# Kernel optimization log

Measured on AMD Instinct MI355X. Metric: run time of the kernel, lower is better.

## Reference

```python
import jax, jax.numpy as jnp
import numpy as np

N, E, G = 20000, 320000, 64
F_IN, H_DIM, HEADS, LAYERS, OUT = 128, 256, 8, 8, 128
HEAD_C = H_DIM // HEADS  # 32
SCALE = 1.0 / np.sqrt(HEAD_C)


def setup_inputs() -> dict:
    key = jax.random.key(0)
    ks = jax.random.split(key, 16)
    s = 0.05
    f32 = jnp.float32
    return {
        "x": jax.random.normal(ks[0], (N, F_IN), f32),
        "edge_index": jax.random.randint(ks[1], (2, E), 0, N),
        "batch": jnp.sort(jax.random.randint(ks[2], (N,), 0, G)),
        "W_init": jax.random.normal(ks[3], (F_IN, H_DIM), f32) * s,
        "b_init": jnp.zeros((H_DIM,), f32),
        "Wq": jax.random.normal(ks[4], (LAYERS, H_DIM, H_DIM), f32) * s,
        "bq": jnp.zeros((LAYERS, H_DIM), f32),
        "Wk": jax.random.normal(ks[5], (LAYERS, H_DIM, H_DIM), f32) * s,
        "bk": jnp.zeros((LAYERS, H_DIM), f32),
        "Wv": jax.random.normal(ks[6], (LAYERS, H_DIM, H_DIM), f32) * s,
        "bv": jnp.zeros((LAYERS, H_DIM), f32),
        "Ws": jax.random.normal(ks[7], (LAYERS, H_DIM, H_DIM), f32) * s,
        "bs": jnp.zeros((LAYERS, H_DIM), f32),
        "Wbeta": jax.random.normal(ks[8], (LAYERS, 3 * H_DIM, 1), f32) * s,
        "ln_g": jnp.ones((LAYERS, H_DIM), f32),
        "ln_b": jnp.zeros((LAYERS, H_DIM), f32),
        "W_final": jax.random.normal(ks[9], (H_DIM, OUT), f32) * s,
        "b_final": jnp.zeros((OUT,), f32),
    }


def _transformer_conv(h, src, dst, Wq, bq, Wk, bk, Wv, bv, Ws, bs, Wbeta):
    # PyG TransformerConv (beta=True, concat=True, eval mode -> no dropout)
    q = (h @ Wq + bq).reshape(N, HEADS, HEAD_C)[dst]   # [E,H,C] query at target
    k = (h @ Wk + bk).reshape(N, HEADS, HEAD_C)[src]   # [E,H,C] key at source
    v = (h @ Wv + bv).reshape(N, HEADS, HEAD_C)[src]   # [E,H,C] value at source
    alpha = jnp.einsum("ehc,ehc->eh", q, k) * SCALE     # [E,H]
    amax = jax.ops.segment_max(alpha, dst, num_segments=N)  # [N,H]
    ex = jnp.exp(alpha - amax[dst])
    denom = jax.ops.segment_sum(ex, dst, num_segments=N)    # [N,H]
    attn = ex / (denom[dst] + 1e-16)                         # [E,H]
    out = jax.ops.segment_sum(v * attn[:, :, None], dst, num_segments=N)
    out = out.reshape(N, H_DIM)
    x_r = h @ Ws + bs                                        # root/skip
    beta = jax.nn.sigmoid(jnp.concatenate([out, x_r, out - x_r], axis=-1) @ Wbeta)  # [N,1]
    return beta * x_r + (1.0 - beta) * out


def _layernorm(x, g, b):
    mu = jnp.mean(x, axis=-1, keepdims=True)
    var = jnp.mean(jnp.square(x - mu), axis=-1, keepdims=True)
    return (x - mu) * jax.lax.rsqrt(var + 1e-5) * g + b


def reference(x, edge_index, batch, W_init, b_init, Wq, bq, Wk, bk, Wv, bv, Ws, bs,
              Wbeta, ln_g, ln_b, W_final, b_final):
    src, dst = edge_index[0], edge_index[1]
    h = x @ W_init + b_init
    for i in range(LAYERS):
        h = _transformer_conv(h, src, dst, Wq[i], bq[i], Wk[i], bk[i],
                              Wv[i], bv[i], Ws[i], bs[i], Wbeta[i])
        h = _layernorm(h, ln_g[i], ln_b[i])
        h = jax.nn.relu(h)
    # global mean pool over graphs
    sums = jax.ops.segment_sum(h, batch, num_segments=G)          # [G,H_DIM]
    cnt = jax.ops.segment_sum(jnp.ones((N,), h.dtype), batch, num_segments=G)
    pooled = sums / jnp.maximum(cnt, 1.0)[:, None]
    return pooled @ W_final + b_final
```

## Files before the change

### kernel.cpp

```cpp
#include <hip/hip_runtime.h>
#include <hip/hip_bf16.h>
#include <math.h>

constexpr int N_NODES  = 20000;
constexpr int M_PAD    = 20096;
constexpr int E_EDGES  = 320000;
constexpr int G_GRAPHS = 64;
constexpr int F_IN     = 128;
constexpr int H_DIM    = 256;
constexpr int LAYERS   = 8;
constexpr float SCALE_ATT = 0.17677669529663687f;

typedef __attribute__((ext_vector_type(8))) short bf16x8;
typedef __attribute__((ext_vector_type(4))) float f32x4;
typedef _Float16 half4 __attribute__((ext_vector_type(4)));
typedef unsigned int u32;

__device__ static inline void gload_lds16(void* lds, const void* g) {
    __builtin_amdgcn_global_load_lds((const __attribute__((address_space(1))) u32*)g,
                                     (__attribute__((address_space(3))) u32*)lds, 16, 0, 0);
}

__global__ void count_kernel(const int* __restrict__ dst, int E, int* __restrict__ counts) {
    int i = blockIdx.x * blockDim.x + threadIdx.x;
    if (i < E) atomicAdd(&counts[dst[i]], 1);
}

__global__ __launch_bounds__(1024) void scan_kernel(const int* __restrict__ counts,
                                                    int* __restrict__ offsets, int n) {
    __shared__ int wsum[16];
    __shared__ int carry_s;
    const int t = threadIdx.x;
    const int lane = t & 63, w = t >> 6;
    if (t == 0) { carry_s = 0; offsets[0] = 0; }
    __syncthreads();
    for (int base = 0; base < n; base += 1024) {
        const int i = base + t;
        const int v = (i < n) ? counts[i] : 0;
        int s = v;
        #pragma unroll
        for (int off = 1; off < 64; off <<= 1) {
            int x = __shfl_up(s, off, 64);
            if (lane >= off) s += x;
        }
        if (lane == 63) wsum[w] = s;
        __syncthreads();
        if (w == 0) {
            int x = (lane < 16) ? wsum[lane] : 0;
            #pragma unroll
            for (int off = 1; off < 16; off <<= 1) {
                int y = __shfl_up(x, off, 64);
                if (lane >= off) x += y;
            }
            if (lane < 16) wsum[lane] = x;
        }
        __syncthreads();
        const int wadd = (w > 0) ? wsum[w - 1] : 0;
        const int inc = carry_s + wadd + s;
        if (i < n) offsets[i + 1] = inc;
        __syncthreads();
        if (t == 1023) carry_s = inc;
        __syncthreads();
    }
}

__global__ void scatter_kernel(const int* __restrict__ src, const int* __restrict__ dst, int E,
                               const int* __restrict__ offsets, int* __restrict__ cursor,
                               int* __restrict__ esrc) {
    int i = blockIdx.x * blockDim.x + threadIdx.x;
    if (i < E) {
        int d = dst[i];
        int pos = atomicAdd(&cursor[d], 1);
        esrc[offsets[d] + pos] = src[i];
    }
}

__global__ __launch_bounds__(256) void wt_layers(
        const float* __restrict__ Wq, const float* __restrict__ Wk,
        const float* __restrict__ Wv, const float* __restrict__ Ws,
        __hip_bfloat16* __restrict__ Whi, __hip_bfloat16* __restrict__ Wlo) {
    const int l = blockIdx.z, z = blockIdx.y;
    const int tk = (blockIdx.x & 7) * 32;
    const int tn = (blockIdx.x >> 3) * 32;
    const float* src = (z == 0 ? Wq : z == 1 ? Wk : z == 2 ? Wv : Ws) + (size_t)l * 65536;
    __shared__ float tile[32][33];
    const int tx = threadIdx.x & 31, ty = threadIdx.x >> 5;
    #pragma unroll
    for (int p = 0; p < 4; ++p)
        tile[ty + p * 8][tx] = src[(size_t)(tk + ty + p * 8) * 256 + tn + tx];
    __syncthreads();
    #pragma unroll
    for (int p = 0; p < 4; ++p) {
        int n = tn + ty + p * 8;
        float v = tile[tx][ty + p * 8];
        size_t o = ((size_t)l * 1024 + z * 256 + n) * 256 + tk + tx;
        __hip_bfloat16 hi = __float2bfloat16(v);
        Whi[o] = hi;
        Wlo[o] = __float2bfloat16(v - __bfloat162float(hi));
    }
}

__global__ __launch_bounds__(256) void wt_init(const float* __restrict__ Wi,
        __hip_bfloat16* __restrict__ Whi, __hip_bfloat16* __restrict__ Wlo) {
    const int tk = (blockIdx.x & 3) * 32;
    const int tn = (blockIdx.x >> 2) * 32;
    __shared__ float tile[32][33];
    const int tx = threadIdx.x & 31, ty = threadIdx.x >> 5;
    #pragma unroll
    for (int p = 0; p < 4; ++p)
        tile[ty + p * 8][tx] = Wi[(size_t)(tk + ty + p * 8) * 256 + tn + tx];
    __syncthreads();
    #pragma unroll
    for (int p = 0; p < 4; ++p) {
        int n = tn + ty + p * 8;
        float v = tile[tx][ty + p * 8];
        size_t o = (size_t)n * 128 + tk + tx;
        __hip_bfloat16 hi = __float2bfloat16(v);
        Whi[o] = hi;
        Wlo[o] = __float2bfloat16(v - __bfloat162float(hi));
    }
}

__global__ __launch_bounds__(256) void bias_cat(const float* __restrict__ bq,
        const float* __restrict__ bk, const float* __restrict__ bv,
        const float* __restrict__ bs, float* __restrict__ bcat) {
    int l = blockIdx.x >> 2, z = blockIdx.x & 3;
    const float* b = (z == 0 ? bq : z == 1 ? bk : z == 2 ? bv : bs) + (size_t)l * 256;
    bcat[(size_t)l * 1024 + z * 256 + threadIdx.x] = b[threadIdx.x];
}

__global__ void conv_hi_lo(const float* __restrict__ src, int n,
                           __hip_bfloat16* __restrict__ hi, __hip_bfloat16* __restrict__ lo) {
    int i = blockIdx.x * blockDim.x + threadIdx.x;
    if (i < n) {
        float v = src[i];
        __hip_bfloat16 h = __float2bfloat16(v);
        hi[i] = h;
        lo[i] = __float2bfloat16(v - __bfloat162float(h));
    }
}

template <int WRITE_MODE>
__global__ __launch_bounds__(256) void gemm_mfma(
        const __hip_bfloat16* __restrict__ Ahi, const __hip_bfloat16* __restrict__ Alo,
        const __hip_bfloat16* __restrict__ Bhi, const __hip_bfloat16* __restrict__ Blo,
        const float* __restrict__ bias, int M, int K,
        float* __restrict__ qs, _Float16* __restrict__ kv,
        __hip_bfloat16* __restrict__ Chi, __hip_bfloat16* __restrict__ Clo) {
    const int t = threadIdx.x;
    const int lane = t & 63, wave = t >> 6;

    const int nwg = gridDim.x * gridDim.y;
    const int lid = blockIdx.y * gridDim.x + blockIdx.x;
    const int qch = nwg >> 3, rch = nwg & 7;
    const int xcd = lid & 7, pos = lid >> 3;
    const int swz = (xcd < rch ? xcd * (qch + 1) : rch * (qch + 1) + (xcd - rch) * qch) + pos;
    const int row0 = (swz / gridDim.x) * 128;
    const int col0 = (swz % gridDim.x) * 128;

    __shared__ __align__(16) __hip_bfloat16 smem[2][4][4096];

    const int ch0 = wave * 64 + lane;
    const int ch1 = ch0 + 256;
    const int rA0 = ch0 >> 2, cA0 = (ch0 & 3) ^ ((rA0 >> 1) & 3);
    const int rA1 = ch1 >> 2, cA1 = (ch1 & 3) ^ ((rA1 >> 1) & 3);
    const size_t gOff0 = (size_t)rA0 * K + cA0 * 8;
    const size_t gOff1 = (size_t)rA1 * K + cA1 * 8;
    const size_t gA0 = (size_t)row0 * K + gOff0, gA1 = (size_t)row0 * K + gOff1;
    const size_t gB0 = (size_t)col0 * K + gOff0, gB1 = (size_t)col0 * K + gOff1;

    const int wr = wave >> 1, wc = wave & 1;
    int offA[4], offB[4];
    #pragma unroll
    for (int f = 0; f < 4; ++f) {
        int ra = wr * 64 + f * 16 + (lane & 15);
        offA[f] = ra * 64 + (((lane >> 4) ^ ((ra >> 1) & 3)) << 4);
        int rb = wc * 64 + f * 16 + (lane & 15);
        offB[f] = rb * 64 + (((lane >> 4) ^ ((rb >> 1) & 3)) << 4);
    }

    f32x4 acc[4][4] = {};
    const int nK = K >> 5;

#define STAGE(BUF, KS) { const size_t ko_ = (size_t)(KS) * 32; \
    gload_lds16((char*)&smem[BUF][0][0] + ch0 * 16, Ahi + gA0 + ko_); \
    gload_lds16((char*)&smem[BUF][0][0] + ch1 * 16, Ahi + gA1 + ko_); \
    gload_lds16((char*)&smem[BUF][1][0] + ch0 * 16, Alo + gA0 + ko_); \
    gload_lds16((char*)&smem[BUF][1][0] + ch1 * 16, Alo + gA1 + ko_); \
    gload_lds16((char*)&smem[BUF][2][0] + ch0 * 16, Bhi + gB0 + ko_); \
    gload_lds16((char*)&smem[BUF][2][0] + ch1 * 16, Bhi + gB1 + ko_); \
    gload_lds16((char*)&smem[BUF][3][0] + ch0 * 16, Blo + gB0 + ko_); \
    gload_lds16((char*)&smem[BUF][3][0] + ch1 * 16, Blo + gB1 + ko_); }

    STAGE(0, 0);
    __syncthreads();
    int cur = 0;
    for (int ks = 0; ks < nK; ++ks) {
        if (ks + 1 < nK) STAGE(cur ^ 1, ks + 1);

        bf16x8 ah[4], al[4], bh[4], bl[4];
        #pragma unroll
        for (int f = 0; f < 4; ++f) {
            ah[f] = *(const bf16x8*)((const char*)&smem[cur][0][0] + offA[f]);
            al[f] = *(const bf16x8*)((const char*)&smem[cur][1][0] + offA[f]);
            bh[f] = *(const bf16x8*)((const char*)&smem[cur][2][0] + offB[f]);
            bl[f] = *(const bf16x8*)((const char*)&smem[cur][3][0] + offB[f]);
        }
        #pragma unroll
        for (int i = 0; i < 4; ++i)
            #pragma unroll
            for (int j = 0; j < 4; ++j) {
                acc[i][j] = __builtin_amdgcn_mfma_f32_16x16x32_bf16(al[i], bh[j], acc[i][j], 0, 0, 0);
                acc[i][j] = __builtin_amdgcn_mfma_f32_16x16x32_bf16(ah[i], bl[j], acc[i][j], 0, 0, 0);
                acc[i][j] = __builtin_amdgcn_mfma_f32_16x16x32_bf16(ah[i], bh[j], acc[i][j], 0, 0, 0);
            }
        __syncthreads();
        cur ^= 1;
    }
#undef STAGE

    const int rb = row0 + wr * 64;
    const int cb = col0 + wc * 64;
    #pragma unroll
    for (int i = 0; i < 4; ++i) {
        #pragma unroll
        for (int j = 0; j < 4; ++j) {
            const int c = cb + j * 16 + (lane & 15);
            const float bz = bias[c];
            #pragma unroll
            for (int rg = 0; rg < 4; ++rg) {
                const int r = rb + i * 16 + (lane >> 4) * 4 + rg;
                if (r < M) {
                    const float v = acc[i][j][rg] + bz;
                    if (WRITE_MODE == 0) {
                        const int sec = c >> 8;
                        if (sec == 0)      qs[(size_t)r * 512 + c] = v * SCALE_ATT;
                        else if (sec == 3) qs[(size_t)r * 512 + c - 512] = v;
                        else               kv[(size_t)r * 512 + c - 256] = (_Float16)v;
                    } else {
                        __hip_bfloat16 hi = __float2bfloat16(v);
                        Chi[(size_t)r * 256 + c] = hi;
                        Clo[(size_t)r * 256 + c] = __float2bfloat16(v - __bfloat162float(hi));
                    }
                }
            }
        }
    }
}

template <int WH>
__global__ __launch_bounds__(256) void node_attn_kernel(
        const float* __restrict__ qs, const _Float16* __restrict__ kv,
        const int* __restrict__ offsets,
        const int* __restrict__ esrc, const float* __restrict__ Wbeta,
        const float* __restrict__ ln_g, const float* __restrict__ ln_b,
        float* __restrict__ h_out,
        __hip_bfloat16* __restrict__ h_hi, __hip_bfloat16* __restrict__ h_lo) {
    const int n = blockIdx.x;
    const int t = threadIdx.x;
    const int lane = t & 63, wave = t >> 6;
    __shared__ int s_src[256];
    __shared__ float s_acc[4][256];
    __shared__ float s_s[4][8];
    __shared__ float red[8];
    __shared__ float s_beta;

    const float4 q4 = reinterpret_cast<const float4*>(qs + (size_t)n * 512)[lane];

    float ssum = 0.f;
    float4 accv = make_float4(0.f, 0.f, 0.f, 0.f);
    const int rs = offsets[n], re = offsets[n + 1];

#define LOADKV(KB, VB, J) { const half4* r_ = reinterpret_cast<const half4*>(kv + (size_t)s_src[(J)] * 512); \
                            KB = r_[lane]; VB = r_[64 + lane]; }
#define STEP(KB, VB) { \
    float p_ = q4.x * (float)KB.x + q4.y * (float)KB.y + q4.z * (float)KB.z + q4.w * (float)KB.w; \
    p_ += __shfl_xor(p_, 1, 8); p_ += __shfl_xor(p_, 2, 8); p_ += __shfl_xor(p_, 4, 8); \
    const float e_ = __expf(p_); \
    ssum += e_; \
    accv.x += e_ * (float)VB.x; \
    accv.y += e_ * (float)VB.y; \
    accv.z += e_ * (float)VB.z; \
    accv.w += e_ * (float)VB.w; }

    for (int base = rs; base < re; base += 256) {
        const int cnt = min(re - base, 256);
        if (t < cnt) s_src[t] = esrc[base + t];
        __syncthreads();

        half4 k0, v0, k1, v1, k2, v2, k3, v3;
        int j = wave;
        if (j      < cnt) LOADKV(k0, v0, j);
        if (j + 4  < cnt) LOADKV(k1, v1, j + 4);
        if (j + 8  < cnt) LOADKV(k2, v2, j + 8);
        if (j + 12 < cnt) LOADKV(k3, v3, j + 12);

        while (j < cnt) {
            STEP(k0, v0); if (j + 16 < cnt) LOADKV(k0, v0, j + 16); j += 4;
            if (j >= cnt) break;
            STEP(k1, v1); if (j + 16 < cnt) LOADKV(k1, v1, j + 16); j += 4;
            if (j >= cnt) break;
            STEP(k2, v2); if (j + 16 < cnt) LOADKV(k2, v2, j + 16); j += 4;
            if (j >= cnt) break;
            STEP(k3, v3); if (j + 16 < cnt) LOADKV(k3, v3, j + 16); j += 4;
        }
        __syncthreads();
    }
#undef LOADKV
#undef STEP

    *reinterpret_cast<float4*>(&s_acc[wave][lane * 4]) = accv;
    if ((lane & 7) == 0) s_s[wave][lane >> 3] = ssum;
    __syncthreads();

    const int hd = t >> 5;
    const float den = s_s[0][hd] + s_s[1][hd] + s_s[2][hd] + s_s[3][hd];
    const float out = (s_acc[0][t] + s_acc[1][t] + s_acc[2][t] + s_acc[3][t]) / (den + 1e-16f);

    const float xr = qs[(size_t)n * 512 + 256 + t];

    float bl = out * (Wbeta[t] + Wbeta[512 + t]) + xr * (Wbeta[256 + t] - Wbeta[512 + t]);
    #pragma unroll
    for (int o = 32; o >= 1; o >>= 1) bl += __shfl_xor(bl, o, 64);
    if ((t & 63) == 0) red[wave] = bl;
    __syncthreads();
    if (t == 0) {
        float v = red[0] + red[1] + red[2] + red[3];
        s_beta = 1.f / (1.f + __expf(-v));
    }
    __syncthreads();
    const float beta = s_beta;
    const float hn = beta * xr + (1.f - beta) * out;

    float r1 = hn;
    #pragma unroll
    for (int o = 32; o >= 1; o >>= 1) r1 += __shfl_xor(r1, o, 64);
    if ((t & 63) == 0) red[4 + wave] = r1;
    __syncthreads();
    const float mu = (red[4] + red[5] + red[6] + red[7]) * (1.f / 256.f);
    const float d = hn - mu;
    float r2 = d * d;
    #pragma unroll
    for (int o = 32; o >= 1; o >>= 1) r2 += __shfl_xor(r2, o, 64);
    if ((t & 63) == 0) red[wave] = r2;
    __syncthreads();
    const float var = (red[0] + red[1] + red[2] + red[3]) * (1.f / 256.f);

    float y = d * rsqrtf(var + 1e-5f) * ln_g[t] + ln_b[t];
    y = fmaxf(y, 0.f);
    if (WH == 1) {
        h_out[(size_t)n * 256 + t] = y;
    } else {
        __hip_bfloat16 hi = __float2bfloat16(y);
        h_hi[(size_t)n * 256 + t] = hi;
        h_lo[(size_t)n * 256 + t] = __float2bfloat16(y - __bfloat162float(hi));
    }
}

constexpr int POOL_N = 32;
__global__ __launch_bounds__(256) void pool_kernel(const float* __restrict__ h,
                                                   const int* __restrict__ batch, int Nn,
                                                   float* __restrict__ sums,
                                                   float* __restrict__ cnt) {
    const int start = blockIdx.x * POOL_N;
    const int end = min(start + POOL_N, Nn);
    if (start >= end) return;
    const int t = threadIdx.x;

    float val[POOL_N];
    #pragma unroll
    for (int i = 0; i < POOL_N; ++i) {
        const int n = start + i;
        val[i] = (n < end) ? h[(size_t)n * 256 + t] : 0.f;
    }

    int cur = batch[start];
    float run = 0.f;
    int c = 0;
    #pragma unroll
    for (int i = 0; i < POOL_N; ++i) {
        const int n = start + i;
        if (n >= end) break;
        const int g = batch[n];
        if (g != cur) {
            atomicAdd(&sums[(size_t)cur * 256 + t], run);
            if (t == 0) atomicAdd(&cnt[cur], (float)c);
            run = 0.f; c = 0; cur = g;
        }
        run += val[i];
        ++c;
    }
    atomicAdd(&sums[(size_t)cur * 256 + t], run);
    if (t == 0) atomicAdd(&cnt[cur], (float)c);
}

__global__ __launch_bounds__(128) void final_kernel(const float* __restrict__ sums,
                                                    const float* __restrict__ cnt,
                                                    const float* __restrict__ Wf,
                                                    const float* __restrict__ bf,
                                                    float* __restrict__ out) {
    const int g = blockIdx.x;
    const int t = threadIdx.x;
    __shared__ float p[256];
    const float c = fmaxf(cnt[g], 1.f);
    for (int i = t; i < 256; i += 128) p[i] = sums[(size_t)g * 256 + i] / c;
    __syncthreads();
    float acc = bf[t];
    #pragma unroll 4
    for (int k = 0; k < 256; ++k) acc += p[k] * Wf[k * 128 + t];
    out[(size_t)g * 128 + t] = acc;
}

extern "C" void kernel_launch(void* const* d_in, const int* in_sizes, int n_in,
                              void* d_out, int out_size, void* d_ws, size_t ws_size,
                              hipStream_t stream) {
    const float* x       = (const float*)d_in[0];
    const int*   eidx    = (const int*)  d_in[1];
    const int*   batch   = (const int*)  d_in[2];
    const float* W_init  = (const float*)d_in[3];
    const float* b_init  = (const float*)d_in[4];
    const float* Wq      = (const float*)d_in[5];
    const float* bq      = (const float*)d_in[6];
    const float* Wk      = (const float*)d_in[7];
    const float* bk      = (const float*)d_in[8];
    const float* Wv      = (const float*)d_in[9];
    const float* bv      = (const float*)d_in[10];
    const float* Ws      = (const float*)d_in[11];
    const float* bs      = (const float*)d_in[12];
    const float* Wbeta   = (const float*)d_in[13];
    const float* ln_g    = (const float*)d_in[14];
    const float* ln_b    = (const float*)d_in[15];
    const float* W_final = (const float*)d_in[16];
    const float* b_final = (const float*)d_in[17];

    const int* e_src = eidx;
    const int* e_dst = eidx + E_EDGES;

    char* p = (char*)d_ws;
    auto alloc = [&](size_t bytes) {
        void* r = (void*)p;
        p += (bytes + 255) & ~(size_t)255;
        return r;
    };
    float* h      = (float*)alloc((size_t)M_PAD * 256 * 4);
    float* qs     = (float*)alloc((size_t)N_NODES * 512 * 4);
    _Float16* kv  = (_Float16*)alloc((size_t)N_NODES * 512 * 2);
    __hip_bfloat16* h_hi = (__hip_bfloat16*)alloc((size_t)M_PAD * 256 * 2);
    __hip_bfloat16* h_lo = (__hip_bfloat16*)alloc((size_t)M_PAD * 256 * 2);
    __hip_bfloat16* x_hi = (__hip_bfloat16*)alloc((size_t)M_PAD * 128 * 2);
    __hip_bfloat16* x_lo = (__hip_bfloat16*)alloc((size_t)M_PAD * 128 * 2);
    __hip_bfloat16* Wt_hi = (__hip_bfloat16*)alloc((size_t)LAYERS * 1024 * 256 * 2);
    __hip_bfloat16* Wt_lo = (__hip_bfloat16*)alloc((size_t)LAYERS * 1024 * 256 * 2);
    __hip_bfloat16* Wi_hi = (__hip_bfloat16*)alloc((size_t)256 * 128 * 2);
    __hip_bfloat16* Wi_lo = (__hip_bfloat16*)alloc((size_t)256 * 128 * 2);
    float* bcat   = (float*)alloc((size_t)LAYERS * 1024 * 4);
    int* counts   = (int*)alloc((size_t)N_NODES * 4);
    int* offsets  = (int*)alloc((size_t)(N_NODES + 1) * 4);
    int* cursor   = (int*)alloc((size_t)N_NODES * 4);
    int* esrc     = (int*)alloc((size_t)E_EDGES * 4);
    float* sums   = (float*)alloc((size_t)G_GRAPHS * 256 * 4);
    float* cnt    = (float*)alloc((size_t)G_GRAPHS * 4);

    hipMemsetAsync(counts, 0, sizeof(int) * N_NODES, stream);
    hipMemsetAsync(cursor, 0, sizeof(int) * N_NODES, stream);
    hipMemsetAsync(sums, 0, sizeof(float) * G_GRAPHS * 256, stream);
    hipMemsetAsync(cnt, 0, sizeof(float) * G_GRAPHS, stream);

    count_kernel<<<(E_EDGES + 255) / 256, 256, 0, stream>>>(e_dst, E_EDGES, counts);
    scan_kernel<<<1, 1024, 0, stream>>>(counts, offsets, N_NODES);
    scatter_kernel<<<(E_EDGES + 255) / 256, 256, 0, stream>>>(e_src, e_dst, E_EDGES,
                                                              offsets, cursor, esrc);

    wt_layers<<<dim3(64, 4, LAYERS), 256, 0, stream>>>(Wq, Wk, Wv, Ws, Wt_hi, Wt_lo);
    wt_init<<<32, 256, 0, stream>>>(W_init, Wi_hi, Wi_lo);
    bias_cat<<<LAYERS * 4, 256, 0, stream>>>(bq, bk, bv, bs, bcat);
    conv_hi_lo<<<(N_NODES * 128 + 255) / 256, 256, 0, stream>>>(x, N_NODES * 128, x_hi, x_lo);

    const int rowTiles = M_PAD / 128;

    gemm_mfma<1><<<dim3(2, rowTiles), 256, 0, stream>>>(
        x_hi, x_lo, Wi_hi, Wi_lo, b_init, N_NODES, 128,
        nullptr, nullptr, h_hi, h_lo);

    for (int l = 0; l < LAYERS; ++l) {
        gemm_mfma<0><<<dim3(8, rowTiles), 256, 0, stream>>>(
            h_hi, h_lo,
            Wt_hi + (size_t)l * 1024 * 256, Wt_lo + (size_t)l * 1024 * 256,
            bcat + (size_t)l * 1024, N_NODES, 256,
            qs, kv, nullptr, nullptr);

        if (l < LAYERS - 1) {
            node_attn_kernel<0><<<N_NODES, 256, 0, stream>>>(
                qs, kv, offsets, esrc,
                Wbeta + (size_t)l * 768,
                ln_g + (size_t)l * 256, ln_b + (size_t)l * 256,
                nullptr, h_hi, h_lo);
        } else {
            node_attn_kernel<1><<<N_NODES, 256, 0, stream>>>(
                qs, kv, offsets, esrc,
                Wbeta + (size_t)l * 768,
                ln_g + (size_t)l * 256, ln_b + (size_t)l * 256,
                h, nullptr, nullptr);
        }
    }

    pool_kernel<<<(N_NODES + POOL_N - 1) / POOL_N, 256, 0, stream>>>(h, batch, N_NODES, sums, cnt);
    final_kernel<<<G_GRAPHS, 128, 0, stream>>>(sums, cnt, W_final, b_final, (float*)d_out);
}
```

Before: 1.123 ms.

## Map one wavefront per node in attention kernel and pipeline GEMM LDS loads

The node attention kernel now gives each wavefront its own node, four nodes per block, instead of spreading one node over a 256-thread block. Edge source indices are read per lane and broadcast with shuffles, so the LDS staging, cross-wave partial-sum reduction and most __syncthreads calls go away. The beta, layernorm and output stores move to float4 vector form. Separately, the GEMM main loop swaps __syncthreads for an explicit vmcnt wait plus s_barrier, so the next tile's global-to-LDS loads can stay in flight while the current tile is computed; this relies on the hand-set wait count matching the number of loads issued per stage.

```diff
diff --git a/kernel.cpp b/kernel.cpp
--- a/kernel.cpp
+++ b/kernel.cpp
@@ -193,10 +193,16 @@
     gload_lds16((char*)&smem[BUF][3][0] + ch1 * 16, Blo + gB1 + ko_); }
 
     STAGE(0, 0);
-    __syncthreads();
     int cur = 0;
     for (int ks = 0; ks < nK; ++ks) {
-        if (ks + 1 < nK) STAGE(cur ^ 1, ks + 1);
+        if (ks + 1 < nK) {
+            STAGE(cur ^ 1, ks + 1);
+            asm volatile("s_waitcnt vmcnt(8)" ::: "memory");
+        } else {
+            asm volatile("s_waitcnt vmcnt(0)" ::: "memory");
+        }
+        __builtin_amdgcn_s_barrier();
+        __builtin_amdgcn_sched_barrier(0);
 
         bf16x8 ah[4], al[4], bh[4], bl[4];
         #pragma unroll
@@ -214,7 +220,8 @@
                 acc[i][j] = __builtin_amdgcn_mfma_f32_16x16x32_bf16(ah[i], bl[j], acc[i][j], 0, 0, 0);
                 acc[i][j] = __builtin_amdgcn_mfma_f32_16x16x32_bf16(ah[i], bh[j], acc[i][j], 0, 0, 0);
             }
-        __syncthreads();
+        __builtin_amdgcn_sched_barrier(0);
+        __builtin_amdgcn_s_barrier();
         cur ^= 1;
     }
 #undef STAGE
@@ -256,104 +263,111 @@
         const float* __restrict__ ln_g, const float* __restrict__ ln_b,
         float* __restrict__ h_out,
         __hip_bfloat16* __restrict__ h_hi, __hip_bfloat16* __restrict__ h_lo) {
-    const int n = blockIdx.x;
     const int t = threadIdx.x;
     const int lane = t & 63, wave = t >> 6;
-    __shared__ int s_src[256];
-    __shared__ float s_acc[4][256];
-    __shared__ float s_s[4][8];
-    __shared__ float red[8];
-    __shared__ float s_beta;
+    const int n = blockIdx.x * 4 + wave;
+    if (n >= N_NODES) return;
 
     const float4 q4 = reinterpret_cast<const float4*>(qs + (size_t)n * 512)[lane];
 
     float ssum = 0.f;
-    float4 accv = make_float4(0.f, 0.f, 0.f, 0.f);
+    float ax = 0.f, ay = 0.f, az = 0.f, aw = 0.f;
     const int rs = offsets[n], re = offsets[n + 1];
 
-#define LOADKV(KB, VB, J) { const half4* r_ = reinterpret_cast<const half4*>(kv + (size_t)s_src[(J)] * 512); \
+#define LOADKV(KB, VB, S) { const half4* r_ = reinterpret_cast<const half4*>(kv + (size_t)(S) * 512); \
                             KB = r_[lane]; VB = r_[64 + lane]; }
 #define STEP(KB, VB) { \
     float p_ = q4.x * (float)KB.x + q4.y * (float)KB.y + q4.z * (float)KB.z + q4.w * (float)KB.w; \
     p_ += __shfl_xor(p_, 1, 8); p_ += __shfl_xor(p_, 2, 8); p_ += __shfl_xor(p_, 4, 8); \
     const float e_ = __expf(p_); \
     ssum += e_; \
-    accv.x += e_ * (float)VB.x; \
-    accv.y += e_ * (float)VB.y; \
-    accv.z += e_ * (float)VB.z; \
-    accv.w += e_ * (float)VB.w; }
-
-    for (int base = rs; base < re; base += 256) {
-        const int cnt = min(re - base, 256);
-        if (t < cnt) s_src[t] = esrc[base + t];
-        __syncthreads();
+    ax += e_ * (float)VB.x; \
+    ay += e_ * (float)VB.y; \
+    az += e_ * (float)VB.z; \
+    aw += e_ * (float)VB.w; }
+
+    for (int base = rs; base < re; base += 64) {
+        const int cnt = min(re - base, 64);
+        const int idx = (lane < cnt) ? esrc[base + lane] : 0;
 
         half4 k0, v0, k1, v1, k2, v2, k3, v3;
-        int j = wave;
-        if (j      < cnt) LOADKV(k0, v0, j);
-        if (j + 4  < cnt) LOADKV(k1, v1, j + 4);
-        if (j + 8  < cnt) LOADKV(k2, v2, j + 8);
-        if (j + 12 < cnt) LOADKV(k3, v3, j + 12);
-
+        if (0 < cnt) LOADKV(k0, v0, __shfl(idx, 0));
+        if (1 < cnt) LOADKV(k1, v1, __shfl(idx, 1));
+        if (2 < cnt) LOADKV(k2, v2, __shfl(idx, 2));
+        if (3 < cnt) LOADKV(k3, v3, __shfl(idx, 3));
+
+        int j = 0;
         while (j < cnt) {
-            STEP(k0, v0); if (j + 16 < cnt) LOADKV(k0, v0, j + 16); j += 4;
+            STEP(k0, v0); if (j + 4 < cnt) LOADKV(k0, v0, __shfl(idx, j + 4)); ++j;
             if (j >= cnt) break;
-            STEP(k1, v1); if (j + 16 < cnt) LOADKV(k1, v1, j + 16); j += 4;
+            STEP(k1, v1); if (j + 4 < cnt) LOADKV(k1, v1, __shfl(idx, j + 4)); ++j;
             if (j >= cnt) break;
-            STEP(k2, v2); if (j + 16 < cnt) LOADKV(k2, v2, j + 16); j += 4;
+            STEP(k2, v2); if (j + 4 < cnt) LOADKV(k2, v2, __shfl(idx, j + 4)); ++j;
             if (j >= cnt) break;
-            STEP(k3, v3); if (j + 16 < cnt) LOADKV(k3, v3, j + 16); j += 4;
-        }
-        __syncthreads();
+            STEP(k3, v3); if (j + 4 < cnt) LOADKV(k3, v3, __shfl(idx, j + 4)); ++j;
+        }
     }
 #undef LOADKV
 #undef STEP
 
-    *reinterpret_cast<float4*>(&s_acc[wave][lane * 4]) = accv;
-    if ((lane & 7) == 0) s_s[wave][lane >> 3] = ssum;
-    __syncthreads();
-
-    const int hd = t >> 5;
-    const float den = s_s[0][hd] + s_s[1][hd] + s_s[2][hd] + s_s[3][hd];
-    const float out = (s_acc[0][t] + s_acc[1][t] + s_acc[2][t] + s_acc[3][t]) / (den + 1e-16f);
-
-    const float xr = qs[(size_t)n * 512 + 256 + t];
-
-    float bl = out * (Wbeta[t] + Wbeta[512 + t]) + xr * (Wbeta[256 + t] - Wbeta[512 + t]);
+    const float inv = 1.f / (ssum + 1e-16f);
+    const float ox = ax * inv, oy = ay * inv, oz = az * inv, ow = aw * inv;
+
+    const float4 xr = reinterpret_cast<const float4*>(qs + (size_t)n * 512 + 256)[lane];
+    const float4 w0 = reinterpret_cast<const float4*>(Wbeta)[lane];
+    const float4 w1 = reinterpret_cast<const float4*>(Wbeta + 256)[lane];
+    const float4 w2 = reinterpret_cast<const float4*>(Wbeta + 512)[lane];
+
+    float bl = ox * (w0.x + w2.x) + xr.x * (w1.x - w2.x)
+             + oy * (w0.y + w2.y) + xr.y * (w1.y - w2.y)
+             + oz * (w0.z + w2.z) + xr.z * (w1.z - w2.z)
+             + ow * (w0.w + w2.w) + xr.w * (w1.w - w2.w);
     #pragma unroll
     for (int o = 32; o >= 1; o >>= 1) bl += __shfl_xor(bl, o, 64);
-    if ((t & 63) == 0) red[wave] = bl;
-    __syncthreads();
-    if (t == 0) {
-        float v = red[0] + red[1] + red[2] + red[3];
-        s_beta = 1.f / (1.f + __expf(-v));
-    }
-    __syncthreads();
-    const float beta = s_beta;
-    const float hn = beta * xr + (1.f - beta) * out;
-
-    float r1 = hn;
-    #pragma unroll
-    for (int o = 32; o >= 1; o >>= 1) r1 += __shfl_xor(r1, o, 64);
-    if ((t & 63) == 0) red[4 + wave] = r1;
-    __syncthreads();
-    const float mu = (red[4] + red[5] + red[6] + red[7]) * (1.f / 256.f);
-    const float d = hn - mu;
-    float r2 = d * d;
-    #pragma unroll
-    for (int o = 32; o >= 1; o >>= 1) r2 += __shfl_xor(r2, o, 64);
-    if ((t & 63) == 0) red[wave] = r2;
-    __syncthreads();
-    const float var = (red[0] + red[1] + red[2] + red[3]) * (1.f / 256.f);
-
-    float y = d * rsqrtf(var + 1e-5f) * ln_g[t] + ln_b[t];
-    y = fmaxf(y, 0.f);
+    const float beta = 1.f / (1.f + __expf(-bl));
+
+    const float hx = beta * xr.x + (1.f - beta) * ox;
+    const float hy = beta * xr.y + (1.f - beta) * oy;
+    const float hz = beta * xr.z + (1.f - beta) * oz;
+    const float hw = beta * xr.w + (1.f - beta) * ow;
+
+    float s1 = hx + hy + hz + hw;
+    #pragma unroll
+    for (int o = 32; o >= 1; o >>= 1) s1 += __shfl_xor(s1, o, 64);
+    const float mu = s1 * (1.f / 256.f);
+
+    const float dx = hx - mu, dy = hy - mu, dz = hz - mu, dw = hw - mu;
+    float s2 = dx * dx + dy * dy + dz * dz + dw * dw;
+    #pragma unroll
+    for (int o = 32; o >= 1; o >>= 1) s2 += __shfl_xor(s2, o, 64);
+    const float rstd = rsqrtf(s2 * (1.f / 256.f) + 1e-5f);
+
+    const float4 g4 = reinterpret_cast<const float4*>(ln_g)[lane];
+    const float4 b4 = reinterpret_cast<const float4*>(ln_b)[lane];
+    float4 y;
+    y.x = fmaxf(dx * rstd * g4.x + b4.x, 0.f);
+    y.y = fmaxf(dy * rstd * g4.y + b4.y, 0.f);
+    y.z = fmaxf(dz * rstd * g4.z + b4.z, 0.f);
+    y.w = fmaxf(dw * rstd * g4.w + b4.w, 0.f);
+
     if (WH == 1) {
-        h_out[(size_t)n * 256 + t] = y;
+        reinterpret_cast<float4*>(h_out + (size_t)n * 256)[lane] = y;
     } else {
-        __hip_bfloat16 hi = __float2bfloat16(y);
-        h_hi[(size_t)n * 256 + t] = hi;
-        h_lo[(size_t)n * 256 + t] = __float2bfloat16(y - __bfloat162float(hi));
+        ushort4 uhi, ulo;
+        __hip_bfloat16 h0 = __float2bfloat16(y.x);
+        __hip_bfloat16 h1 = __float2bfloat16(y.y);
+        __hip_bfloat16 h2 = __float2bfloat16(y.z);
+        __hip_bfloat16 h3 = __float2bfloat16(y.w);
+        __hip_bfloat16 l0 = __float2bfloat16(y.x - __bfloat162float(h0));
+        __hip_bfloat16 l1 = __float2bfloat16(y.y - __bfloat162float(h1));
+        __hip_bfloat16 l2 = __float2bfloat16(y.z - __bfloat162float(h2));
+        __hip_bfloat16 l3 = __float2bfloat16(y.w - __bfloat162float(h3));
+        uhi.x = *(unsigned short*)&h0; uhi.y = *(unsigned short*)&h1;
+        uhi.z = *(unsigned short*)&h2; uhi.w = *(unsigned short*)&h3;
+        ulo.x = *(unsigned short*)&l0; ulo.y = *(unsigned short*)&l1;
+        ulo.z = *(unsigned short*)&l2; ulo.w = *(unsigned short*)&l3;
+        reinterpret_cast<ushort4*>(h_hi + (size_t)n * 256)[lane] = uhi;
+        reinterpret_cast<ushort4*>(h_lo + (size_t)n * 256)[lane] = ulo;
     }
 }
 
@@ -490,13 +504,13 @@
             qs, kv, nullptr, nullptr);
 
         if (l < LAYERS - 1) {
-            node_attn_kernel<0><<<N_NODES, 256, 0, stream>>>(
+            node_attn_kernel<0><<<(N_NODES + 3) / 4, 256, 0, stream>>>(
                 qs, kv, offsets, esrc,
                 Wbeta + (size_t)l * 768,
                 ln_g + (size_t)l * 256, ln_b + (size_t)l * 256,
                 nullptr, h_hi, h_lo);
         } else {
-            node_attn_kernel<1><<<N_NODES, 256, 0, stream>>>(
+            node_attn_kernel<1><<<(N_NODES + 3) / 4, 256, 0, stream>>>(
                 qs, kv, offsets, esrc,
                 Wbeta + (size_t)l * 768,
                 ln_g + (size_t)l * 256, ln_b + (size_t)l * 256,
```

Measured after the change: 1.078 ms. 1.04x faster.
